# Performance work log

Measured on AMD Instinct MI355X. Metric: run time of the kernel, lower is better.

The kernel has to match this reference:

```python
import jax, jax.numpy as jnp
import numpy as np

B, T, C = 4, 2048, 2048
N_HEAD, N_HEAD_KV = 16, 4
HEAD_DIM = C // N_HEAD
ROPE_BASE = 10000.0


def setup_inputs() -> dict:
    key = jax.random.key(0)
    ks = jax.random.split(key, 6)
    x = jax.random.normal(ks[0], (B, T, C), dtype=jnp.float32)
    # freqs_cis: (T, head_dim//2, 2) with [...,0]=cos, [...,1]=sin (true RoPE angles)
    inv_freq = 1.0 / (ROPE_BASE ** (jnp.arange(0, HEAD_DIM, 2, dtype=jnp.float32) / HEAD_DIM))
    angles = jnp.arange(T, dtype=jnp.float32)[:, None] * inv_freq[None, :]  # (T, hd//2)
    freqs_cis = jnp.stack([jnp.cos(angles), jnp.sin(angles)], axis=-1)
    s = 0.02
    Wq = jax.random.normal(ks[1], (C, C), dtype=jnp.float32) * s
    Wk = jax.random.normal(ks[2], (N_HEAD_KV * HEAD_DIM, C), dtype=jnp.float32) * s
    Wv = jax.random.normal(ks[3], (N_HEAD_KV * HEAD_DIM, C), dtype=jnp.float32) * s
    Wo = jax.random.normal(ks[4], (C, C), dtype=jnp.float32) * s
    return {"x": x, "freqs_cis": freqs_cis, "Wq": Wq, "Wk": Wk, "Wv": Wv, "Wo": Wo}


def _rotate_half(u):
    h = u.shape[-1] // 2
    return jnp.concatenate([-u[..., h:], u[..., :h]], axis=-1)


def reference(x, freqs_cis, Wq, Wk, Wv, Wo):
    b, t, c = x.shape
    hd = HEAD_DIM
    q = (x @ Wq.T).reshape(b, t, N_HEAD, hd)
    k = (x @ Wk.T).reshape(b, t, N_HEAD_KV, hd)
    v = (x @ Wv.T).reshape(b, t, N_HEAD_KV, hd)
    # external RoPE (3-dim freqs_cis): cos/sin repeated to full head_dim
    cos = freqs_cis[:t, :, 0]
    sin = freqs_cis[:t, :, 1]
    cos = jnp.concatenate([cos, cos], axis=-1)[None, :, None, :]  # (1,T,1,hd)
    sin = jnp.concatenate([sin, sin], axis=-1)[None, :, None, :]
    q = q * cos + _rotate_half(q) * sin
    k = k * cos + _rotate_half(k) * sin
    # GQA: repeat_interleave kv heads to n_head
    g = N_HEAD // N_HEAD_KV
    k = jnp.repeat(k, g, axis=2)  # (B,T,H,hd)
    v = jnp.repeat(v, g, axis=2)
    scale = 1.0 / np.sqrt(hd)
    scores = jnp.einsum('bthd,bshd->bhts', q, k) * scale  # (B,H,T,S)
    causal = jnp.tril(jnp.ones((t, t), dtype=bool))
    neg = jnp.finfo(scores.dtype).min
    scores = jnp.where(causal[None, None, :, :], scores, neg)
    attn = jax.nn.softmax(scores, axis=-1)
    out = jnp.einsum('bhts,bshd->bthd', attn, v).reshape(b, t, c)
    return out @ Wo.T
```

## Files before the change

kernel.cpp:

```cpp
#include <hip/hip_runtime.h>
#include <hip/hip_bf16.h>
#include <stdint.h>

typedef __bf16 bf16_t;
typedef __bf16 bf16x4 __attribute__((ext_vector_type(4)));
typedef __bf16 bf16x8 __attribute__((ext_vector_type(8)));
typedef float f32x4 __attribute__((ext_vector_type(4)));

__device__ __forceinline__ float fast_exp2(float x) {
#if __has_builtin(__builtin_amdgcn_exp2f)
  return __builtin_amdgcn_exp2f(x);
#else
  return exp2f(x);
#endif
}

__global__ void cvt_f32_bf16(const float* __restrict__ in, bf16_t* __restrict__ out, int n4) {
  int i = blockIdx.x * blockDim.x + threadIdx.x;
  if (i >= n4) return;
  float4 v = ((const float4*)in)[i];
  bf16x4 o = { (bf16_t)v.x, (bf16_t)v.y, (bf16_t)v.z, (bf16_t)v.w };
  *(bf16x4*)(out + (size_t)i * 4) = o;
}

__device__ __forceinline__ void async_load16(const bf16_t* g, bf16_t* l) {
#if __has_builtin(__builtin_amdgcn_global_load_lds)
  __builtin_amdgcn_global_load_lds((const __attribute__((address_space(1))) void*)g,
                                   (__attribute__((address_space(3))) void*)l, 16, 0, 0);
#else
  *(bf16x8*)l = *(const bf16x8*)g;
#endif
}

template<bool F32OUT>
__global__ __launch_bounds__(256) void gemm_bt(const bf16_t* __restrict__ A,
                                               const bf16_t* __restrict__ B,
                                               void* __restrict__ C,
                                               int M, int N, int K) {
  __shared__ bf16_t Alds[128 * 64];
  __shared__ bf16_t Blds[128 * 64];
  const int tid = threadIdx.x;
  const int wave = tid >> 6, lane = tid & 63;
  const int lrow = lane & 15, quad = lane >> 4;
  const int wr = wave >> 1, wc = wave & 1;
  const int bm = blockIdx.y, bn = blockIdx.x;
  const bf16_t* Ab = A + (size_t)bm * 128 * K;
  const bf16_t* Bb = B + (size_t)bn * 128 * K;
  const int r0 = tid >> 3;
  const int c0 = ((tid & 7) ^ (r0 & 7)) << 3;
  f32x4 acc[4][4] = {};

  for (int kk = 0; kk < K; kk += 64) {
#pragma unroll
    for (int p = 0; p < 4; ++p) {
      async_load16(Ab + (size_t)(p * 32 + r0) * K + kk + c0, &Alds[(p * 256 + tid) * 8]);
      async_load16(Bb + (size_t)(p * 32 + r0) * K + kk + c0, &Blds[(p * 256 + tid) * 8]);
    }
    __syncthreads();
#pragma unroll
    for (int ks2 = 0; ks2 < 2; ++ks2) {
      const int rc = ((ks2 * 4 + quad) ^ (lrow & 7)) << 3;
      bf16x8 af[4], bfv[4];
#pragma unroll
      for (int mt = 0; mt < 4; ++mt)
        af[mt] = *(const bf16x8*)&Alds[(wr * 64 + mt * 16 + lrow) * 64 + rc];
#pragma unroll
      for (int nt = 0; nt < 4; ++nt)
        bfv[nt] = *(const bf16x8*)&Blds[(wc * 64 + nt * 16 + lrow) * 64 + rc];
#pragma unroll
      for (int mt = 0; mt < 4; ++mt)
#pragma unroll
        for (int nt = 0; nt < 4; ++nt)
          acc[mt][nt] = __builtin_amdgcn_mfma_f32_16x16x32_bf16(af[mt], bfv[nt], acc[mt][nt], 0, 0, 0);
    }
    __syncthreads();
  }

#pragma unroll
  for (int mt = 0; mt < 4; ++mt)
#pragma unroll
    for (int nt = 0; nt < 4; ++nt)
#pragma unroll
      for (int r = 0; r < 4; ++r) {
        int row = bm * 128 + wr * 64 + mt * 16 + quad * 4 + r;
        int col = bn * 128 + wc * 64 + nt * 16 + lrow;
        if (F32OUT) ((float*)C)[(size_t)row * N + col] = acc[mt][nt][r];
        else        ((bf16_t*)C)[(size_t)row * N + col] = (bf16_t)acc[mt][nt][r];
      }
}

__global__ void rope_kernel(bf16_t* __restrict__ X, const float* __restrict__ F,
                            int hshift, int stride) {
  int i = blockIdx.x * blockDim.x + threadIdx.x;
  int d = i & 63;
  int h = (i >> 6) & ((1 << hshift) - 1);
  int row = i >> (6 + hshift);
  int t = row & 2047;
  float c = F[t * 128 + d * 2];
  float s = F[t * 128 + d * 2 + 1];
  size_t base = (size_t)row * stride + h * 128 + d;
  float q0 = (float)X[base];
  float q1 = (float)X[base + 64];
  X[base]      = (bf16_t)(q0 * c - q1 * s);
  X[base + 64] = (bf16_t)(q1 * c + q0 * s);
}

__global__ __launch_bounds__(256) void transpose_v(const bf16_t* __restrict__ KV,
                                                   bf16_t* __restrict__ Vt) {
  __shared__ bf16_t tile[64][72];
  const int tid = threadIdx.x;
  const int t0 = blockIdx.x * 64;
  const int c0 = blockIdx.y * 64;
#pragma unroll
  for (int p = 0; p < 4; ++p) {
    int idx = p * 256 + tid;
    int r = idx >> 4, c4 = (idx & 15) * 4;
    *(bf16x4*)&tile[r][c4] = *(const bf16x4*)&KV[(size_t)(t0 + r) * 3072 + 2560 + c0 + c4];
  }
  __syncthreads();
  const int bb = t0 >> 11, t0b = t0 & 2047;
#pragma unroll
  for (int p = 0; p < 4; ++p) {
    int idx = p * 256 + tid;
    int cr = idx >> 4, t4 = (idx & 15) * 4;
    int c = c0 + cr;
    int R = (bb * 4 + (c >> 7)) * 128 + (c & 127);
    bf16x4 o;
#pragma unroll
    for (int j = 0; j < 4; ++j) o[j] = tile[t4 + j][cr];
    *(bf16x4*)&Vt[(size_t)R * 2048 + t0b + t4] = o;
  }
}

__global__ __launch_bounds__(256, 2) void attn_kernel(const bf16_t* __restrict__ QKV,
                                                      const float* __restrict__ F,
                                                      const bf16_t* __restrict__ Vt,
                                                      bf16_t* __restrict__ O) {
  __shared__ bf16_t Ks[64 * 128];
  __shared__ bf16_t Vs[128 * 64];
  __shared__ bf16_t Ps[4 * 32 * 72];
  const int tid = threadIdx.x;
  const int wave = tid >> 6, lane = tid & 63;
  const int lrow = lane & 15, quad = lane >> 4;
  const int bh = blockIdx.y, b = bh >> 4, h = bh & 15, kvh = h >> 2;
  const size_t qoff  = ((size_t)b * 2048) * 3072 + (size_t)h * 128;
  const size_t koff  = ((size_t)b * 2048) * 3072 + 2048 + (size_t)kvh * 128;
  const size_t vtoff = ((size_t)(b * 4 + kvh) * 128) * 2048;
  const float qsc = 0.08838834764831845f * 1.44269504088896340736f;
  bf16_t* Pw = Ps + wave * (32 * 72);
  const float2* F2 = (const float2*)F;

  const int krow_l = tid >> 4;
  const int kdc    = (tid & 15) ^ (krow_l & 7);
  const int vrow_l = tid >> 3;
  const int vkc    = (tid & 7) ^ (vrow_l & 7);

  for (int phase = 0; phase < 2; ++phase) {
    const int qt = phase ? (15 - blockIdx.x) : blockIdx.x;
    const int qbase = qt * 128 + wave * 32;

    bf16x8 qf[2][4];
#pragma unroll
    for (int nt2 = 0; nt2 < 2; ++nt2) {
      const int t = qbase + nt2 * 16 + lrow;
      const bf16_t* qp = QKV + qoff + (size_t)t * 3072 + quad * 8;
      bf16x8 raw[4];
#pragma unroll
      for (int ks = 0; ks < 4; ++ks) raw[ks] = *(const bf16x8*)(qp + ks * 32);
#pragma unroll
      for (int ks2 = 0; ks2 < 2; ++ks2) {
        bf16x8 lo, hi;
#pragma unroll
        for (int j = 0; j < 8; ++j) {
          int d = ks2 * 32 + quad * 8 + j;
          float2 cs = F2[t * 64 + d];
          float q0 = (float)raw[ks2][j], q1 = (float)raw[ks2 + 2][j];
          lo[j] = (bf16_t)((q0 * cs.x - q1 * cs.y) * qsc);
          hi[j] = (bf16_t)((q1 * cs.x + q0 * cs.y) * qsc);
        }
        qf[nt2][ks2]     = lo;
        qf[nt2][ks2 + 2] = hi;
      }
    }

    f32x4 Oacc[2][8] = {};
    float m_r[2] = {-1.0e30f, -1.0e30f};
    float l_r[2] = {0.f, 0.f};
    const int kt_end = 2 * qt + 2;

    for (int kt = 0; kt < kt_end; ++kt) {
      __syncthreads();
      const bf16_t* Kg = QKV + koff + (size_t)(kt * 64) * 3072;
      const bf16_t* Vg = Vt + vtoff + kt * 64;
#pragma unroll
      for (int c4 = 0; c4 < 4; ++c4) {
        int ci = c4 * 256 + tid;
        async_load16(Kg + (size_t)(c4 * 16 + krow_l) * 3072 + kdc * 8, &Ks[ci * 8]);
        async_load16(Vg + (size_t)(c4 * 32 + vrow_l) * 2048 + vkc * 8, &Vs[ci * 8]);
      }
      __syncthreads();

      if (kt * 64 <= qbase + 31) {
        f32x4 S[2][4] = {};
#pragma unroll
        for (int ks = 0; ks < 4; ++ks) {
          bf16x8 kf[4];
#pragma unroll
          for (int mt = 0; mt < 4; ++mt) {
            int dc = (ks * 4 + quad) ^ (lrow & 7);
            kf[mt] = *(const bf16x8*)&Ks[(mt * 16 + lrow) * 128 + dc * 8];
          }
#pragma unroll
          for (int nt2 = 0; nt2 < 2; ++nt2)
#pragma unroll
            for (int mt = 0; mt < 4; ++mt)
              S[nt2][mt] = __builtin_amdgcn_mfma_f32_16x16x32_bf16(kf[mt], qf[nt2][ks], S[nt2][mt], 0, 0, 0);
        }
        if (kt * 64 + 63 > qbase) {
#pragma unroll
          for (int nt2 = 0; nt2 < 2; ++nt2) {
            int q = qbase + nt2 * 16 + lrow;
#pragma unroll
            for (int mt = 0; mt < 4; ++mt) {
              int key0 = kt * 64 + mt * 16 + quad * 4;
#pragma unroll
              for (int r = 0; r < 4; ++r)
                if (key0 + r > q) S[nt2][mt][r] = -1.0e30f;
            }
          }
        }
        float alpha[2];
#pragma unroll
        for (int nt2 = 0; nt2 < 2; ++nt2) {
          float mx = -1.0e30f;
#pragma unroll
          for (int mt = 0; mt < 4; ++mt)
#pragma unroll
            for (int r = 0; r < 4; ++r) mx = fmaxf(mx, S[nt2][mt][r]);
          mx = fmaxf(mx, __shfl_xor(mx, 16, 64));
          mx = fmaxf(mx, __shfl_xor(mx, 32, 64));
          float mnew = fmaxf(m_r[nt2], mx);
          alpha[nt2] = fast_exp2(m_r[nt2] - mnew);
          m_r[nt2] = mnew;
          float rs = 0.f;
#pragma unroll
          for (int mt = 0; mt < 4; ++mt) {
            bf16x4 pk;
#pragma unroll
            for (int r = 0; r < 4; ++r) {
              float p = fast_exp2(S[nt2][mt][r] - mnew);
              rs += p;
              pk[r] = (bf16_t)p;
            }
            *(bf16x4*)&Pw[(nt2 * 16 + lrow) * 72 + mt * 16 + quad * 4] = pk;
          }
          rs += __shfl_xor(rs, 16, 64);
          rs += __shfl_xor(rs, 32, 64);
          l_r[nt2] = l_r[nt2] * alpha[nt2] + rs;
        }
        bool nz = (alpha[0] != 1.f) || (alpha[1] != 1.f);
        if (__ballot(nz) != 0ull) {
#pragma unroll
          for (int mt2 = 0; mt2 < 2; ++mt2)
#pragma unroll
            for (int r = 0; r < 4; ++r) {
              float av = __shfl(alpha[mt2], quad * 4 + r, 16);
#pragma unroll
              for (int dt = 0; dt < 8; ++dt) Oacc[mt2][dt][r] *= av;
            }
        }
#pragma unroll
        for (int ks2 = 0; ks2 < 2; ++ks2) {
          bf16x8 ap[2];
#pragma unroll
          for (int mt2 = 0; mt2 < 2; ++mt2)
            ap[mt2] = *(const bf16x8*)&Pw[(mt2 * 16 + lrow) * 72 + ks2 * 32 + quad * 8];
          int dc = (ks2 * 4 + quad) ^ (lrow & 7);
#pragma unroll
          for (int dt = 0; dt < 8; ++dt) {
            bf16x8 bv = *(const bf16x8*)&Vs[(dt * 16 + lrow) * 64 + dc * 8];
#pragma unroll
            for (int mt2 = 0; mt2 < 2; ++mt2)
              Oacc[mt2][dt] = __builtin_amdgcn_mfma_f32_16x16x32_bf16(ap[mt2], bv, Oacc[mt2][dt], 0, 0, 0);
          }
        }
      }
    }

#pragma unroll
    for (int mt2 = 0; mt2 < 2; ++mt2)
#pragma unroll
      for (int r = 0; r < 4; ++r) {
        float lv = __shfl(l_r[mt2], quad * 4 + r, 16);
        float inv = 1.0f / lv;
        int row = qbase + mt2 * 16 + quad * 4 + r;
#pragma unroll
        for (int dt = 0; dt < 8; ++dt)
          O[(size_t)(bh >> 4) * 2048 * 2048 + (size_t)row * 2048 + (bh & 15) * 128 + dt * 16 + lrow] =
              (bf16_t)(Oacc[mt2][dt][r] * inv);
      }
  }
}

extern "C" void kernel_launch(void* const* d_in, const int* in_sizes, int n_in,
                              void* d_out, int out_size, void* d_ws, size_t ws_size,
                              hipStream_t stream) {
  const float* x  = (const float*)d_in[0];
  const float* fc = (const float*)d_in[1];
  const float* Wq = (const float*)d_in[2];
  const float* Wk = (const float*)d_in[3];
  const float* Wv = (const float*)d_in[4];
  const float* Wo = (const float*)d_in[5];
  float* out = (float*)d_out;

  char* ws = (char*)d_ws;
  size_t off = 0;
  auto alloc = [&](size_t bytes) { char* p = ws + off; off += bytes; return p; };
  bf16_t* xb    = (bf16_t*)alloc((size_t)8192 * 2048 * 2);
  bf16_t* Wqkvb = (bf16_t*)alloc((size_t)3072 * 2048 * 2);
  bf16_t* Wob   = (bf16_t*)alloc((size_t)2048 * 2048 * 2);
  bf16_t* QKVb  = (bf16_t*)alloc((size_t)8192 * 3072 * 2);
  bf16_t* Ab    = (bf16_t*)alloc((size_t)8192 * 2048 * 2);
  bf16_t* Vtb   = xb;
  (void)ws_size; (void)in_sizes; (void)n_in; (void)out_size;

  cvt_f32_bf16<<<16384, 256, 0, stream>>>(x,  xb, 4194304);
  cvt_f32_bf16<<<4096,  256, 0, stream>>>(Wq, Wqkvb, 1048576);
  cvt_f32_bf16<<<1024,  256, 0, stream>>>(Wk, Wqkvb + (size_t)2048 * 2048, 262144);
  cvt_f32_bf16<<<1024,  256, 0, stream>>>(Wv, Wqkvb + (size_t)2560 * 2048, 262144);
  cvt_f32_bf16<<<4096,  256, 0, stream>>>(Wo, Wob, 1048576);

  gemm_bt<false><<<dim3(24, 64), 256, 0, stream>>>(xb, Wqkvb, QKVb, 8192, 3072, 2048);

  rope_kernel<<<8192, 256, 0, stream>>>(QKVb + 2048, fc, 2, 3072);

  transpose_v<<<dim3(128, 8), 256, 0, stream>>>(QKVb, Vtb);

  attn_kernel<<<dim3(8, 64), 256, 0, stream>>>(QKVb, fc, Vtb, Ab);

  gemm_bt<true><<<dim3(16, 64), 256, 0, stream>>>(Ab, Wob, out, 8192, 2048, 2048);
}
```

Baseline: 462.2 us.

## Fuse conversions, write V transposed from QKV GEMM, double-buffer attention K/V

Merges the five f32-to-bf16 conversion launches into one kernel and drops the separate V transpose kernel by having the QKV GEMM epilogue write V columns directly in transposed layout, which shrinks the QKV buffer to 2560 columns. The attention kernel now double-buffers K/V tiles in LDS so the next tile's loads are issued before the current tile is computed. The P scratch buffer moves from padded rows to an XOR-swizzled layout. These changes cut launches, one global round trip for V, and load-wait stalls, at the cost of more LDS per block, which may reduce occupancy.

```diff
diff --git a/kernel.cpp b/kernel.cpp
--- a/kernel.cpp
+++ b/kernel.cpp
@@ -15,12 +15,20 @@
 #endif
 }
 
-__global__ void cvt_f32_bf16(const float* __restrict__ in, bf16_t* __restrict__ out, int n4) {
-  int i = blockIdx.x * blockDim.x + threadIdx.x;
-  if (i >= n4) return;
-  float4 v = ((const float4*)in)[i];
+__global__ void cvt_all(const float* __restrict__ x,  const float* __restrict__ Wq,
+                        const float* __restrict__ Wk, const float* __restrict__ Wv,
+                        const float* __restrict__ Wo, bf16_t* __restrict__ xb,
+                        bf16_t* __restrict__ wqkv, bf16_t* __restrict__ wob) {
+  const int bid = blockIdx.x, tid = threadIdx.x;
+  const float* src; bf16_t* dst; int i;
+  if (bid < 16384)      { src = x;  dst = xb;             i = bid * 256 + tid; }
+  else if (bid < 20480) { src = Wq; dst = wqkv;           i = (bid - 16384) * 256 + tid; }
+  else if (bid < 21504) { src = Wk; dst = wqkv + 4194304; i = (bid - 20480) * 256 + tid; }
+  else if (bid < 22528) { src = Wv; dst = wqkv + 5242880; i = (bid - 21504) * 256 + tid; }
+  else                  { src = Wo; dst = wob;            i = (bid - 22528) * 256 + tid; }
+  float4 v = ((const float4*)src)[i];
   bf16x4 o = { (bf16_t)v.x, (bf16_t)v.y, (bf16_t)v.z, (bf16_t)v.w };
-  *(bf16x4*)(out + (size_t)i * 4) = o;
+  *(bf16x4*)(dst + (size_t)i * 4) = o;
 }
 
 __device__ __forceinline__ void async_load16(const bf16_t* g, bf16_t* l) {
@@ -32,11 +40,12 @@
 #endif
 }
 
-template<bool F32OUT>
+template<bool F32OUT, bool VSPLIT>
 __global__ __launch_bounds__(256) void gemm_bt(const bf16_t* __restrict__ A,
                                                const bf16_t* __restrict__ B,
                                                void* __restrict__ C,
-                                               int M, int N, int K) {
+                                               bf16_t* __restrict__ Vt,
+                                               int M, int N, int K, int ldc) {
   __shared__ bf16_t Alds[128 * 64];
   __shared__ bf16_t Blds[128 * 64];
   const int tid = threadIdx.x;
@@ -76,6 +85,21 @@
     __syncthreads();
   }
 
+  if (VSPLIT && bn >= 20) {
+#pragma unroll
+    for (int mt = 0; mt < 4; ++mt)
+#pragma unroll
+      for (int nt = 0; nt < 4; ++nt) {
+        int row = bm * 128 + wr * 64 + mt * 16 + quad * 4;
+        int cv  = bn * 128 + wc * 64 + nt * 16 + lrow - 2560;
+        int b = row >> 11, tl = row & 2047;
+        bf16x4 o;
+#pragma unroll
+        for (int r = 0; r < 4; ++r) o[r] = (bf16_t)acc[mt][nt][r];
+        *(bf16x4*)&Vt[((size_t)(b * 512 + cv)) * 2048 + tl] = o;
+      }
+    return;
+  }
 #pragma unroll
   for (int mt = 0; mt < 4; ++mt)
 #pragma unroll
@@ -84,8 +108,8 @@
       for (int r = 0; r < 4; ++r) {
         int row = bm * 128 + wr * 64 + mt * 16 + quad * 4 + r;
         int col = bn * 128 + wc * 64 + nt * 16 + lrow;
-        if (F32OUT) ((float*)C)[(size_t)row * N + col] = acc[mt][nt][r];
-        else        ((bf16_t*)C)[(size_t)row * N + col] = (bf16_t)acc[mt][nt][r];
+        if (F32OUT) ((float*)C)[(size_t)row * ldc + col] = acc[mt][nt][r];
+        else        ((bf16_t*)C)[(size_t)row * ldc + col] = (bf16_t)acc[mt][nt][r];
       }
 }
 
@@ -105,49 +129,22 @@
   X[base + 64] = (bf16_t)(q1 * c + q0 * s);
 }
 
-__global__ __launch_bounds__(256) void transpose_v(const bf16_t* __restrict__ KV,
-                                                   bf16_t* __restrict__ Vt) {
-  __shared__ bf16_t tile[64][72];
-  const int tid = threadIdx.x;
-  const int t0 = blockIdx.x * 64;
-  const int c0 = blockIdx.y * 64;
-#pragma unroll
-  for (int p = 0; p < 4; ++p) {
-    int idx = p * 256 + tid;
-    int r = idx >> 4, c4 = (idx & 15) * 4;
-    *(bf16x4*)&tile[r][c4] = *(const bf16x4*)&KV[(size_t)(t0 + r) * 3072 + 2560 + c0 + c4];
-  }
-  __syncthreads();
-  const int bb = t0 >> 11, t0b = t0 & 2047;
-#pragma unroll
-  for (int p = 0; p < 4; ++p) {
-    int idx = p * 256 + tid;
-    int cr = idx >> 4, t4 = (idx & 15) * 4;
-    int c = c0 + cr;
-    int R = (bb * 4 + (c >> 7)) * 128 + (c & 127);
-    bf16x4 o;
-#pragma unroll
-    for (int j = 0; j < 4; ++j) o[j] = tile[t4 + j][cr];
-    *(bf16x4*)&Vt[(size_t)R * 2048 + t0b + t4] = o;
-  }
-}
-
 __global__ __launch_bounds__(256, 2) void attn_kernel(const bf16_t* __restrict__ QKV,
                                                       const float* __restrict__ F,
                                                       const bf16_t* __restrict__ Vt,
                                                       bf16_t* __restrict__ O) {
-  __shared__ bf16_t Ks[64 * 128];
-  __shared__ bf16_t Vs[128 * 64];
-  __shared__ bf16_t Ps[4 * 32 * 72];
+  __shared__ bf16_t Ks[2][64 * 128];
+  __shared__ bf16_t Vs[2][128 * 64];
+  __shared__ bf16_t Ps[4 * 32 * 64];
   const int tid = threadIdx.x;
   const int wave = tid >> 6, lane = tid & 63;
   const int lrow = lane & 15, quad = lane >> 4;
   const int bh = blockIdx.y, b = bh >> 4, h = bh & 15, kvh = h >> 2;
-  const size_t qoff  = ((size_t)b * 2048) * 3072 + (size_t)h * 128;
-  const size_t koff  = ((size_t)b * 2048) * 3072 + 2048 + (size_t)kvh * 128;
+  const size_t qoff  = ((size_t)b * 2048) * 2560 + (size_t)h * 128;
+  const size_t koff  = ((size_t)b * 2048) * 2560 + 2048 + (size_t)kvh * 128;
   const size_t vtoff = ((size_t)(b * 4 + kvh) * 128) * 2048;
   const float qsc = 0.08838834764831845f * 1.44269504088896340736f;
-  bf16_t* Pw = Ps + wave * (32 * 72);
+  bf16_t* Pw = Ps + wave * (32 * 64);
   const float2* F2 = (const float2*)F;
 
   const int krow_l = tid >> 4;
@@ -155,6 +152,19 @@
   const int vrow_l = tid >> 3;
   const int vkc    = (tid & 7) ^ (vrow_l & 7);
 
+  auto stage = [&](int kt, int bsel) {
+    const bf16_t* Kg = QKV + koff + (size_t)(kt * 64) * 2560;
+    const bf16_t* Vg = Vt + vtoff + kt * 64;
+    bf16_t* Kd = &Ks[bsel][0];
+    bf16_t* Vd = &Vs[bsel][0];
+#pragma unroll
+    for (int c4 = 0; c4 < 4; ++c4) {
+      int ci = c4 * 256 + tid;
+      async_load16(Kg + (size_t)(c4 * 16 + krow_l) * 2560 + kdc * 8, Kd + ci * 8);
+      async_load16(Vg + (size_t)(c4 * 32 + vrow_l) * 2048 + vkc * 8, Vd + ci * 8);
+    }
+  };
+
   for (int phase = 0; phase < 2; ++phase) {
     const int qt = phase ? (15 - blockIdx.x) : blockIdx.x;
     const int qbase = qt * 128 + wave * 32;
@@ -163,7 +173,7 @@
 #pragma unroll
     for (int nt2 = 0; nt2 < 2; ++nt2) {
       const int t = qbase + nt2 * 16 + lrow;
-      const bf16_t* qp = QKV + qoff + (size_t)t * 3072 + quad * 8;
+      const bf16_t* qp = QKV + qoff + (size_t)t * 2560 + quad * 8;
       bf16x8 raw[4];
 #pragma unroll
       for (int ks = 0; ks < 4; ++ks) raw[ks] = *(const bf16x8*)(qp + ks * 32);
@@ -188,17 +198,13 @@
     float l_r[2] = {0.f, 0.f};
     const int kt_end = 2 * qt + 2;
 
+    stage(0, 0);
+
     for (int kt = 0; kt < kt_end; ++kt) {
       __syncthreads();
-      const bf16_t* Kg = QKV + koff + (size_t)(kt * 64) * 3072;
-      const bf16_t* Vg = Vt + vtoff + kt * 64;
-#pragma unroll
-      for (int c4 = 0; c4 < 4; ++c4) {
-        int ci = c4 * 256 + tid;
-        async_load16(Kg + (size_t)(c4 * 16 + krow_l) * 3072 + kdc * 8, &Ks[ci * 8]);
-        async_load16(Vg + (size_t)(c4 * 32 + vrow_l) * 2048 + vkc * 8, &Vs[ci * 8]);
-      }
-      __syncthreads();
+      if (kt + 1 < kt_end) stage(kt + 1, (kt + 1) & 1);
+      const bf16_t* Kb_ = &Ks[kt & 1][0];
+      const bf16_t* Vb_ = &Vs[kt & 1][0];
 
       if (kt * 64 <= qbase + 31) {
         f32x4 S[2][4] = {};
@@ -208,7 +214,7 @@
 #pragma unroll
           for (int mt = 0; mt < 4; ++mt) {
             int dc = (ks * 4 + quad) ^ (lrow & 7);
-            kf[mt] = *(const bf16x8*)&Ks[(mt * 16 + lrow) * 128 + dc * 8];
+            kf[mt] = *(const bf16x8*)&Kb_[(mt * 16 + lrow) * 128 + dc * 8];
           }
 #pragma unroll
           for (int nt2 = 0; nt2 < 2; ++nt2)
@@ -243,6 +249,8 @@
           alpha[nt2] = fast_exp2(m_r[nt2] - mnew);
           m_r[nt2] = mnew;
           float rs = 0.f;
+          const int prow = nt2 * 16 + lrow;
+          const int pbase = prow * 64 + ((quad & 1) << 2);
 #pragma unroll
           for (int mt = 0; mt < 4; ++mt) {
             bf16x4 pk;
@@ -252,7 +260,8 @@
               rs += p;
               pk[r] = (bf16_t)p;
             }
-            *(bf16x4*)&Pw[(nt2 * 16 + lrow) * 72 + mt * 16 + quad * 4] = pk;
+            int c8 = ((mt * 2 + (quad >> 1)) ^ (prow & 7)) << 3;
+            *(bf16x4*)&Pw[pbase + c8] = pk;
           }
           rs += __shfl_xor(rs, 16, 64);
           rs += __shfl_xor(rs, 32, 64);
@@ -273,12 +282,14 @@
         for (int ks2 = 0; ks2 < 2; ++ks2) {
           bf16x8 ap[2];
 #pragma unroll
-          for (int mt2 = 0; mt2 < 2; ++mt2)
-            ap[mt2] = *(const bf16x8*)&Pw[(mt2 * 16 + lrow) * 72 + ks2 * 32 + quad * 8];
+          for (int mt2 = 0; mt2 < 2; ++mt2) {
+            int prow = mt2 * 16 + lrow;
+            ap[mt2] = *(const bf16x8*)&Pw[prow * 64 + (((ks2 * 4 + quad) ^ (prow & 7)) << 3)];
+          }
           int dc = (ks2 * 4 + quad) ^ (lrow & 7);
 #pragma unroll
           for (int dt = 0; dt < 8; ++dt) {
-            bf16x8 bv = *(const bf16x8*)&Vs[(dt * 16 + lrow) * 64 + dc * 8];
+            bf16x8 bv = *(const bf16x8*)&Vb_[(dt * 16 + lrow) * 64 + dc * 8];
 #pragma unroll
             for (int mt2 = 0; mt2 < 2; ++mt2)
               Oacc[mt2][dt] = __builtin_amdgcn_mfma_f32_16x16x32_bf16(ap[mt2], bv, Oacc[mt2][dt], 0, 0, 0);
@@ -296,7 +307,7 @@
         int row = qbase + mt2 * 16 + quad * 4 + r;
 #pragma unroll
         for (int dt = 0; dt < 8; ++dt)
-          O[(size_t)(bh >> 4) * 2048 * 2048 + (size_t)row * 2048 + (bh & 15) * 128 + dt * 16 + lrow] =
+          O[(size_t)b * 2048 * 2048 + (size_t)row * 2048 + h * 128 + dt * 16 + lrow] =
               (bf16_t)(Oacc[mt2][dt][r] * inv);
       }
   }
@@ -319,24 +330,20 @@
   bf16_t* xb    = (bf16_t*)alloc((size_t)8192 * 2048 * 2);
   bf16_t* Wqkvb = (bf16_t*)alloc((size_t)3072 * 2048 * 2);
   bf16_t* Wob   = (bf16_t*)alloc((size_t)2048 * 2048 * 2);
-  bf16_t* QKVb  = (bf16_t*)alloc((size_t)8192 * 3072 * 2);
+  bf16_t* QKVb  = (bf16_t*)alloc((size_t)8192 * 2560 * 2);
   bf16_t* Ab    = (bf16_t*)alloc((size_t)8192 * 2048 * 2);
-  bf16_t* Vtb   = xb;
+  bf16_t* Vtb   = (bf16_t*)alloc((size_t)2048 * 2048 * 2);
   (void)ws_size; (void)in_sizes; (void)n_in; (void)out_size;
 
-  cvt_f32_bf16<<<16384, 256, 0, stream>>>(x,  xb, 4194304);
-  cvt_f32_bf16<<<4096,  256, 0, stream>>>(Wq, Wqkvb, 1048576);
-  cvt_f32_bf16<<<1024,  256, 0, stream>>>(Wk, Wqkvb + (size_t)2048 * 2048, 262144);
-  cvt_f32_bf16<<<1024,  256, 0, stream>>>(Wv, Wqkvb + (size_t)2560 * 2048, 262144);
-  cvt_f32_bf16<<<4096,  256, 0, stream>>>(Wo, Wob, 1048576);
-
-  gemm_bt<false><<<dim3(24, 64), 256, 0, stream>>>(xb, Wqkvb, QKVb, 8192, 3072, 2048);
-
-  rope_kernel<<<8192, 256, 0, stream>>>(QKVb + 2048, fc, 2, 3072);
-
-  transpose_v<<<dim3(128, 8), 256, 0, stream>>>(QKVb, Vtb);
+  cvt_all<<<26624, 256, 0, stream>>>(x, Wq, Wk, Wv, Wo, xb, Wqkvb, Wob);
+
+  gemm_bt<false, true><<<dim3(24, 64), 256, 0, stream>>>(xb, Wqkvb, QKVb, Vtb,
+                                                         8192, 3072, 2048, 2560);
+
+  rope_kernel<<<8192, 256, 0, stream>>>(QKVb + 2048, fc, 2, 2560);
 
   attn_kernel<<<dim3(8, 64), 256, 0, stream>>>(QKVb, fc, Vtb, Ab);
 
-  gemm_bt<true><<<dim3(16, 64), 256, 0, stream>>>(Ab, Wob, out, 8192, 2048, 2048);
-}
+  gemm_bt<true, false><<<dim3(16, 64), 256, 0, stream>>>(Ab, Wob, out, nullptr,
+                                                         8192, 2048, 2048, 2048);
+}
```

After: 460.7 us. Within noise of the previous version (-0.3%).
